# Kernel optimization log

Measured on AMD Instinct MI355X. Metric: run time of the kernel, lower is better.

Reference implementation:

```python
import jax, jax.numpy as jnp
import numpy as np

ALPHA = 0.01
EPSB = ALPHA / (1.0 - 2.0 * ALPHA)  # boundary_eps
BIG = 1e9  # stands in for +inf; all real boundary distances are << box diameter


def setup_inputs() -> dict:
    key = jax.random.key(0)
    ks = jax.random.split(key, 8)
    B, D, K = 32768, 16, 1024
    return {
        "x": jax.random.normal(ks[0], (B, D), jnp.float32),
        "logp": jnp.zeros((B, 1), jnp.float32),
        "an1_w": 0.1 * jax.random.normal(ks[1], (D,), jnp.float32),
        "an1_b": 0.1 * jax.random.normal(ks[2], (D,), jnp.float32),
        "an2_w": 0.1 * jax.random.normal(ks[3], (D,), jnp.float32),
        "an2_b": 0.1 * jax.random.normal(ks[4], (D,), jnp.float32),
        "shift_coeff": jax.random.normal(ks[5], (D,), jnp.float32),
        "anchor_raw": jax.random.normal(ks[6], (1, K, D), jnp.float32),  # vorproj._anchor_pts
        "box_min": -4.0 * jnp.ones((D,), jnp.float32),
        "box_max": 4.0 * jnp.ones((D,), jnp.float32),
        "mixture_logits": jnp.zeros((K,), jnp.float32),
    }


def reference(x, logp, an1_w, an1_b, an2_w, an2_b, shift_coeff,
              anchor_raw, box_min, box_max, mixture_logits):
    B, D = x.shape
    # --- actnorm1: y = (x + b) * exp(w); logdet = sum(w) ---
    x = (x + an1_b) * jnp.exp(an1_w)
    logp = logp - jnp.sum(an1_w)
    # --- logit_transform.inverse: y = (sigmoid(x) - alpha) / (1 - 2*alpha) ---
    ld = jnp.sum(jax.nn.log_sigmoid(x) + jax.nn.log_sigmoid(-x), axis=1, keepdims=True) \
         - D * jnp.log(1.0 - 2.0 * ALPHA)
    x = (jax.nn.sigmoid(x) - ALPHA) / (1.0 - 2.0 * ALPHA)
    logp = logp - ld
    # --- (-eps, 1+eps) -> (0, 1) ---
    span = 1.0 + 2.0 * EPSB
    x = (x + EPSB) / span
    logp = logp + D * jnp.log(span)
    # --- scale into box constraints ---
    scale = box_max - box_min  # (D,)
    x = x * scale + box_min
    logp = logp - jnp.sum(jnp.log(scale))
    # --- anchor points: R -> (-1,1) -> (0,1) -> box ---
    a = anchor_raw[0]                       # (K, D)
    a = a / (1.0 + jnp.abs(a))
    a = (a + 1.0) * 0.5 * scale + box_min   # (K, D)
    K = a.shape[0]
    # --- find_nearest: argmin_k ||x - a_k||^2 (drop const ||x||^2) ---
    a_sq = jnp.sum(a * a, axis=1)                    # (K,)
    d2 = a_sq[None, :] - 2.0 * (x @ a.T)             # (B, K)
    k = jnp.argmin(d2, axis=1)                       # (B,)
    mask = jax.nn.one_hot(k, K, dtype=bool).reshape(B, 1, K)
    x_k = a[k]                                       # (B, D) gathered anchor
    # --- shift toward anchor: x + c*(x_k - x); logdet = sum log(1-c) ---
    c = jax.nn.sigmoid(shift_coeff) * 0.98 + 0.01
    x = x + c * (x_k - x)
    logp = logp - jnp.sum(jnp.log1p(-c))
    # --- map_outside_cell: radial map of Voronoi cell (within box) onto R^D ---
    dx = x - x_k
    r = jnp.sqrt(jnp.sum(dx * dx, axis=1))           # (B,)
    u = dx / jnp.maximum(r, 1e-12)[:, None]          # (B, D) unit direction
    # half-plane boundary distance t_j = (||a_j - a_k||^2 / 2) / (u . (a_j - a_k))
    proj = u @ a.T - jnp.sum(u * x_k, axis=1, keepdims=True)              # (B, K)
    halfdist = 0.5 * (a_sq[None, :] + a_sq[k][:, None] - 2.0 * (x_k @ a.T))  # (B, K)
    self_mask = jnp.arange(K)[None, :] == k[:, None]
    valid = jnp.logical_and(jnp.logical_not(self_mask), proj > 1e-12)
    t_half = jnp.where(valid, halfdist / jnp.where(valid, proj, 1.0), BIG)
    # box-face distances along u
    up = u > 1e-12
    un = u < -1e-12
    t_box = jnp.where(up, (box_max[None, :] - x_k) / jnp.where(up, u, 1.0),
            jnp.where(un, (box_min[None, :] - x_k) / jnp.where(un, u, 1.0), BIG))
    t = jnp.minimum(jnp.min(t_half, axis=1), jnp.min(t_box, axis=1))      # (B,)
    ratio = r / t                                     # in [0, 0.99] after shift
    s = 1.0 / (1.0 - ratio)
    x = x_k + dx * s[:, None]
    # logdet = (D+1) * log(t / (t - r)) = -(D+1) * log1p(-ratio)
    logp = logp + (D + 1.0) * jnp.log1p(-ratio)[:, None]
    # --- subtract cell center ---
    x = x - x_k
    # --- actnorm2 ---
    x = (x + an2_b) * jnp.exp(an2_w)
    logp = logp - jnp.sum(an2_w)
    # --- mixture component log-prob ---
    logprobs = jax.nn.log_softmax(mixture_logits)
    logp = logp - logprobs[k][:, None]
    return x, logp, mask
```

## Files before the change

kernel.cpp:

```cpp
#include <hip/hip_runtime.h>
#include <math.h>

#define DD 16
#define KK 1024

#define WS_A    0
#define WS_ASQ  16384
#define WS_OMC  17408
#define WS_B2   17424
#define WS_E2   17440
#define WS_MN   17456
#define WS_MX   17472
#define WS_SCL  17488
#define WS_DIM  17504
#define WS_E1   17520
#define WS_BASE 17536
#define WS_TOTD 17537
#define WS_NEED_BYTES (WS_TOTD * 8)

__device__ __forceinline__ double xformD(double rv, double mn, double scl) {
  double t = rv / (1.0 + fabs(rv));
  return (t + 1.0) * 0.5 * scl + mn;
}
__device__ __forceinline__ float xformF(float v, float mn, float mx) {
  return (v / (1.f + fabsf(v)) + 1.f) * 0.5f * (mx - mn) + mn;
}

__global__ __launch_bounds__(256) void vor_pre(
    const float* __restrict__ an1_w, const float* __restrict__ an2_w,
    const float* __restrict__ an2_b, const float* __restrict__ shift_c,
    const float* __restrict__ anchor_raw,
    const float* __restrict__ box_min, const float* __restrict__ box_max,
    const float* __restrict__ mlogits, double* __restrict__ ws)
{
  __shared__ double redD[16];
  const int tid = threadIdx.x;
  const int blk = blockIdx.x;

  if (blk == 0 && tid < DD) {
    double w1 = (double)an1_w[tid], w2 = (double)an2_w[tid];
    double sgc = 1.0 / (1.0 + exp(-(double)shift_c[tid]));
    double c = sgc * 0.98 + 0.01;
    double mn = (double)box_min[tid], mx = (double)box_max[tid];
    ws[WS_OMC + tid] = 1.0 - c;
    ws[WS_B2  + tid] = (double)an2_b[tid];
    ws[WS_E2  + tid] = exp(w2);
    ws[WS_MN  + tid] = mn;
    ws[WS_MX  + tid] = mx;
    ws[WS_SCL + tid] = mx - mn;
    ws[WS_E1  + tid] = exp(w1);
    ws[WS_DIM + tid] = -w1 - log(mx - mn) - log1p(-c) - w2;
  }
  const int j0 = blk * 64;
  for (int e = tid; e < 64 * DD; e += 256) {
    int j = j0 + (e >> 4), d = e & 15;
    double mn = (double)box_min[d];
    double scl = (double)box_max[d] - mn;
    ws[WS_A + (size_t)j * DD + d] = xformD((double)anchor_raw[j * DD + d], mn, scl);
  }
  __syncthreads();
  for (int j = j0 + tid; j < j0 + 64; j += 256) {
    double s = 0.0;
    #pragma unroll
    for (int d = 0; d < DD; ++d) { double a = ws[WS_A + (size_t)j * DD + d]; s = fma(a, a, s); }
    ws[WS_ASQ + j] = s;
  }
  if (blk != 0) return;
  float lm = -3.4e38f;
  for (int i = tid; i < KK; i += 256) lm = fmaxf(lm, mlogits[i]);
  #pragma unroll
  for (int o = 32; o > 0; o >>= 1) lm = fmaxf(lm, __shfl_xor(lm, o));
  if ((tid & 63) == 0) redD[tid >> 6] = (double)lm;
  __syncthreads();
  float gmax = (float)fmax(fmax(redD[0], redD[1]), fmax(redD[2], redD[3]));
  double lsum = 0.0;
  for (int i = tid; i < KK; i += 256) lsum += exp((double)mlogits[i] - (double)gmax);
  #pragma unroll
  for (int o = 32; o > 0; o >>= 1) lsum += __shfl_xor(lsum, o);
  if ((tid & 63) == 0) redD[4 + (tid >> 6)] = lsum;
  __syncthreads();
  if (tid == 0) {
    double lse = (double)gmax + log(redD[4] + redD[5] + redD[6] + redD[7]);
    double b = (double)DD * (log(0.98) + log(1.0 + 2.0 * (0.01 / 0.98)));
    #pragma unroll
    for (int d = 0; d < DD; ++d) b += ws[WS_DIM + d];
    ws[WS_BASE] = b + lse;
  }
}

#define NT2 1024
#define RPB2 128
#define SL2 8
#define JSL2 (KK / SL2)

__global__ __launch_bounds__(NT2, 4) void vor4(
    const float* __restrict__ x_in, const float* __restrict__ logp_in,
    const float* __restrict__ an1_b,
    const float* __restrict__ mlogits, const double* __restrict__ ws,
    float* __restrict__ out, int Brows)
{
  __shared__ __align__(16) float sA[KK][DD];
  __shared__ float  sAsqH[KK];
  __shared__ double sX4D[DD][RPB2];
  __shared__ float  sLT[DD][RPB2];
  __shared__ double sD2[16][64];
  __shared__ int    sJJ[16][64];
  __shared__ float  sRat[16][64];
  __shared__ float  sOmcF[DD], sB2F[DD], sE2F[DD], sMnF[DD], sMxF[DD];

  const int tid  = threadIdx.x;
  const int w    = tid >> 6;
  const int lane = tid & 63;
  const int rg   = w >> 3;
  const int sl   = w & 7;
  const int rrow = rg * 64 + lane;
  const int row  = blockIdx.x * RPB2 + rrow;
  const size_t coreEnd = (size_t)Brows * (DD + 1);

  if (tid < DD) {
    sOmcF[tid] = (float)ws[WS_OMC + tid];
    sB2F[tid]  = (float)ws[WS_B2 + tid];
    sE2F[tid]  = (float)ws[WS_E2 + tid];
    sMnF[tid]  = (float)ws[WS_MN + tid];
    sMxF[tid]  = (float)ws[WS_MX + tid];
  }
  for (int e = tid; e < KK * DD / 4; e += NT2) {
    double2 p0 = ((const double2*)(ws + WS_A))[e * 2 + 0];
    double2 p1 = ((const double2*)(ws + WS_A))[e * 2 + 1];
    ((float4*)sA)[e] = make_float4((float)p0.x, (float)p0.y, (float)p1.x, (float)p1.y);
  }
  {
    const double A = 0.01, EPSB = 0.01 / 0.98;
    const double SPAN = 1.0 + 2.0 * EPSB;
    const float* xb = x_in + (size_t)blockIdx.x * RPB2 * DD;
    for (int e = tid; e < RPB2 * DD; e += NT2) {
      int rr = e >> 4, d = e & 15;
      double y1 = ((double)xb[e] + (double)an1_b[d]) * ws[WS_E1 + d];
      double sg = 1.0 / (1.0 + exp(-y1));
      double x2 = (sg - A) / (1.0 - 2.0 * A);
      double x3 = (x2 + EPSB) / SPAN;
      double x4 = x3 * ws[WS_SCL + d] + ws[WS_MN + d];
      sX4D[d][rr] = x4;
      double ay = fabs(y1);
      sLT[d][rr] = (float)(ay + 2.0 * log1p(exp(-ay)));
    }
  }
  {
    float4* mz = (float4*)(out + coreEnd + (size_t)blockIdx.x * RPB2 * KK);
    #pragma unroll 4
    for (int i = tid; i < RPB2 * KK / 4; i += NT2)
      mz[i] = make_float4(0.f, 0.f, 0.f, 0.f);
  }
  __syncthreads();

  for (int j = tid; j < KK; j += NT2) {
    float acc = 0.f;
    #pragma unroll
    for (int d = 0; d < DD; ++d) { float a = sA[j][d]; acc = fmaf(a, a, acc); }
    sAsqH[j] = 0.5f * acc;
  }

  float x4f[DD];
  #pragma unroll
  for (int d = 0; d < DD; ++d) x4f[d] = (float)sX4D[d][rrow];
  __syncthreads();

  const int jlo = sl * JSL2, jhi = jlo + JSL2;
  float m1 = -3.4e38f, m2v = -3.4e38f;
  int j1 = jlo, j2v = jlo;
  #pragma unroll 4
  for (int j = jlo; j < jhi; ++j) {
    const float4* ar = (const float4*)&sA[j][0];
    float4 a0 = ar[0], a1 = ar[1], a2 = ar[2], a3 = ar[3];
    float accA = -sAsqH[j], accB = 0.f;
    accA = fmaf(x4f[0],  a0.x, accA); accB = fmaf(x4f[8],  a2.x, accB);
    accA = fmaf(x4f[1],  a0.y, accA); accB = fmaf(x4f[9],  a2.y, accB);
    accA = fmaf(x4f[2],  a0.z, accA); accB = fmaf(x4f[10], a2.z, accB);
    accA = fmaf(x4f[3],  a0.w, accA); accB = fmaf(x4f[11], a2.w, accB);
    accA = fmaf(x4f[4],  a1.x, accA); accB = fmaf(x4f[12], a3.x, accB);
    accA = fmaf(x4f[5],  a1.y, accA); accB = fmaf(x4f[13], a3.y, accB);
    accA = fmaf(x4f[6],  a1.z, accA); accB = fmaf(x4f[14], a3.z, accB);
    accA = fmaf(x4f[7],  a1.w, accA); accB = fmaf(x4f[15], a3.w, accB);
    float acc = accA + accB;
    bool gt1 = acc > m1;
    bool gt2 = acc > m2v;
    m2v = gt1 ? m1 : (gt2 ? acc : m2v);
    j2v = gt1 ? j1 : (gt2 ? j : j2v);
    m1  = gt1 ? acc : m1;
    j1  = gt1 ? j : j1;
  }

  {
    double bestD = 1e300; int bk = 0x7fffffff;
    #pragma unroll
    for (int t = 0; t < 2; ++t) {
      int j = t ? j2v : j1;
      const double* aj = ws + WS_A + (size_t)j * DD;
      double dot = 0.0;
      #pragma unroll
      for (int d = 0; d < DD; ++d) dot = fma(sX4D[d][rrow], aj[d], dot);
      double d2 = ws[WS_ASQ + j] - 2.0 * dot;
      if (d2 < bestD || (d2 == bestD && j < bk)) { bestD = d2; bk = j; }
    }
    sD2[w][lane] = bestD;
    sJJ[w][lane] = bk;
  }
  __syncthreads();

  int k = 0x7fffffff;
  {
    double kb = 1e300;
    #pragma unroll
    for (int ss = 0; ss < SL2; ++ss) {
      double d = sD2[rg * 8 + ss][lane];
      int    j = sJJ[rg * 8 + ss][lane];
      if (d < kb || (d == kb && j < k)) { kb = d; k = j; }
    }
  }

  float akf[DD], dxf[DD];
  float r2f = 0.f, dxak = 0.f;
  #pragma unroll
  for (int d = 0; d < DD; ++d) {
    float a = sA[k][d];
    akf[d] = a;
    float dx = sOmcF[d] * (x4f[d] - a);
    dxf[d] = dx;
    r2f  = fmaf(dx, dx, r2f);
    dxak = fmaf(dx, a, dxak);
  }
  const float rf   = sqrtf(r2f);
  const float rrf  = fmaxf(rf, 1e-12f);
  const float scal = rf / rrf;
  const float epsr = 1e-12f * rf;
  const float asqhk = sAsqH[k];

  float q1 = 0.f, h1 = 1.f;
  #pragma unroll 2
  for (int j = jlo; j < jhi; ++j) {
    const float4* ar = (const float4*)&sA[j][0];
    float4 a0 = ar[0], a1 = ar[1], a2 = ar[2], a3 = ar[3];
    float qA = -dxak, qB = 0.f;
    float hA = asqhk + sAsqH[j], hB = 0.f;
    qA = fmaf(dxf[0],  a0.x, qA); qB = fmaf(dxf[8],  a2.x, qB);
    hA = fmaf(-akf[0], a0.x, hA); hB = fmaf(-akf[8], a2.x, hB);
    qA = fmaf(dxf[1],  a0.y, qA); qB = fmaf(dxf[9],  a2.y, qB);
    hA = fmaf(-akf[1], a0.y, hA); hB = fmaf(-akf[9], a2.y, hB);
    qA = fmaf(dxf[2],  a0.z, qA); qB = fmaf(dxf[10], a2.z, qB);
    hA = fmaf(-akf[2], a0.z, hA); hB = fmaf(-akf[10],a2.z, hB);
    qA = fmaf(dxf[3],  a0.w, qA); qB = fmaf(dxf[11], a2.w, qB);
    hA = fmaf(-akf[3], a0.w, hA); hB = fmaf(-akf[11],a2.w, hB);
    qA = fmaf(dxf[4],  a1.x, qA); qB = fmaf(dxf[12], a3.x, qB);
    hA = fmaf(-akf[4], a1.x, hA); hB = fmaf(-akf[12],a3.x, hB);
    qA = fmaf(dxf[5],  a1.y, qA); qB = fmaf(dxf[13], a3.y, qB);
    hA = fmaf(-akf[5], a1.y, hA); hB = fmaf(-akf[13],a3.y, hB);
    qA = fmaf(dxf[6],  a1.z, qA); qB = fmaf(dxf[14], a3.z, qB);
    hA = fmaf(-akf[6], a1.z, hA); hB = fmaf(-akf[14],a3.z, hB);
    qA = fmaf(dxf[7],  a1.w, qA); qB = fmaf(dxf[15], a3.w, qB);
    hA = fmaf(-akf[7], a1.w, hA); hB = fmaf(-akf[15],a3.w, hB);
    float q = qA + qB, h = hA + hB;
    bool upd = (j != k) & (q > epsr) & (q * h1 > q1 * h);
    q1 = upd ? q : q1;
    h1 = upd ? h : h1;
  }
  sRat[w][lane] = scal * (q1 / h1);
  __syncthreads();

  if (sl == 0) {
    float ratio = rf * 1e-9f;
    #pragma unroll
    for (int ss = 0; ss < SL2; ++ss) ratio = fmaxf(ratio, sRat[rg * 8 + ss][lane]);
    #pragma unroll
    for (int d = 0; d < DD; ++d) {
      float uf = dxf[d] / rrf;
      if (uf > 1e-12f)        ratio = fmaxf(ratio, rf * uf / (sMxF[d] - akf[d]));
      else if (uf < -1e-12f)  ratio = fmaxf(ratio, rf * uf / (sMnF[d] - akf[d]));
    }
    float sS = 1.0f / (1.0f - ratio);
    float xo[DD];
    float lsig = 0.f;
    #pragma unroll
    for (int d = 0; d < DD; ++d) {
      xo[d] = (dxf[d] * sS + sB2F[d]) * sE2F[d];
      lsig += sLT[d][rrow];
    }
    float4* xp = (float4*)(out + (size_t)row * DD);
    xp[0] = make_float4(xo[0], xo[1], xo[2], xo[3]);
    xp[1] = make_float4(xo[4], xo[5], xo[6], xo[7]);
    xp[2] = make_float4(xo[8], xo[9], xo[10], xo[11]);
    xp[3] = make_float4(xo[12], xo[13], xo[14], xo[15]);
    double lp = (double)logp_in[row] + ws[WS_BASE] + (double)lsig
              + 17.0 * log1p(-(double)ratio)
              - (double)mlogits[k];
    out[(size_t)Brows * DD + row] = (float)lp;
    out[coreEnd + (size_t)row * KK + k] = 1.0f;
  }
}

#define NT 256
#define RPB 64
#define SLC4 4
#define JSL4 (KK / SLC4)

__global__ __launch_bounds__(NT, 2) void vor_green(
    const float* __restrict__ x_in, const float* __restrict__ logp_in,
    const float* __restrict__ an1_w, const float* __restrict__ an1_b,
    const float* __restrict__ an2_w, const float* __restrict__ an2_b,
    const float* __restrict__ shift_c, const float* __restrict__ anchor_raw,
    const float* __restrict__ box_min, const float* __restrict__ box_max,
    const float* __restrict__ mlogits,
    float* __restrict__ out, int Brows)
{
  __shared__ __align__(16) float sA[KK][DD];
  __shared__ float  sAsqH[KK];
  __shared__ float  sX4T[DD][RPB];
  __shared__ int    sPj1[SLC4][RPB], sPj2[SLC4][RPB];
  __shared__ int    sRI1[SLC4][RPB], sRI2[SLC4][RPB];
  __shared__ double sPartD[8];
  __shared__ double sE1D[DD], sB1D[DD], sOmcD[DD], sB2D[DD], sE2D[DD];
  __shared__ double sMnD[DD], sMxD[DD], sSclD[DD], sDimD[DD];
  __shared__ double sBaseD;
  __shared__ int    sKidx[RPB];

  const int tid  = threadIdx.x;
  const int sl   = tid >> 6;
  const int lane = tid & 63;
  const int row  = blockIdx.x * RPB + lane;
  const size_t coreEnd = (size_t)Brows * (DD + 1);

  for (int e = tid; e < KK * DD / 4; e += NT) {
    float4 raw = ((const float4*)anchor_raw)[e];
    float4 bmn = ((const float4*)box_min)[e & 3];
    float4 bmx = ((const float4*)box_max)[e & 3];
    float4 o;
    o.x = xformF(raw.x, bmn.x, bmx.x);
    o.y = xformF(raw.y, bmn.y, bmx.y);
    o.z = xformF(raw.z, bmn.z, bmx.z);
    o.w = xformF(raw.w, bmn.w, bmx.w);
    ((float4*)sA)[e] = o;
  }
  if (tid < DD) {
    double w1 = (double)an1_w[tid];
    sE1D[tid] = exp(w1);
    sB1D[tid] = (double)an1_b[tid];
    double sgc = 1.0 / (1.0 + exp(-(double)shift_c[tid]));
    double c = sgc * 0.98 + 0.01;
    sOmcD[tid] = 1.0 - c;
    double mn = (double)box_min[tid], mx = (double)box_max[tid];
    sMnD[tid] = mn; sMxD[tid] = mx; sSclD[tid] = mx - mn;
    double w2 = (double)an2_w[tid];
    sE2D[tid] = exp(w2);
    sB2D[tid] = (double)an2_b[tid];
    sDimD[tid] = -w1 - log(mx - mn) - log1p(-c) - w2;
  }
  __syncthreads();

  for (int j = tid; j < KK; j += NT) {
    float acc = 0.f;
    #pragma unroll
    for (int d = 0; d < DD; ++d) { float a = sA[j][d]; acc = fmaf(a, a, acc); }
    sAsqH[j] = 0.5f * acc;
  }

  float lm = -3.4e38f;
  for (int i = tid; i < KK; i += NT) lm = fmaxf(lm, mlogits[i]);
  #pragma unroll
  for (int o = 32; o > 0; o >>= 1) lm = fmaxf(lm, __shfl_xor(lm, o));
  if (lane == 0) sPartD[sl] = (double)lm;
  __syncthreads();
  float gmax = (float)fmax(fmax(sPartD[0], sPartD[1]), fmax(sPartD[2], sPartD[3]));
  double lsum = 0.0;
  for (int i = tid; i < KK; i += NT) lsum += exp((double)mlogits[i] - (double)gmax);
  #pragma unroll
  for (int o = 32; o > 0; o >>= 1) lsum += __shfl_xor(lsum, o);
  if (lane == 0) sPartD[4 + sl] = lsum;
  __syncthreads();
  if (tid == 0) {
    double lse = (double)gmax + log(sPartD[4] + sPartD[5] + sPartD[6] + sPartD[7]);
    double b = (double)DD * (log(0.98) + log(1.0 + 2.0 * (0.01 / 0.98)));
    #pragma unroll
    for (int d = 0; d < DD; ++d) b += sDimD[d];
    sBaseD = b + lse;
  }

  double x4d[DD];
  double lsigD = 0.0;
  if (sl == 0) {
    const double A = 0.01, EPSB = 0.01 / 0.98;
    const double SPAN = 1.0 + 2.0 * EPSB;
    const float* xr = x_in + (size_t)row * DD;
    #pragma unroll
    for (int d = 0; d < DD; ++d) {
      double y1 = ((double)xr[d] + sB1D[d]) * sE1D[d];
      double sg = 1.0 / (1.0 + exp(-y1));
      double x2 = (sg - A) / (1.0 - 2.0 * A);
      double x3 = (x2 + EPSB) / SPAN;
      double x4 = x3 * sSclD[d] + sMnD[d];
      x4d[d] = x4;
      sX4T[d][lane] = (float)x4;
      double ay = fabs(y1);
      lsigD += ay + 2.0 * log1p(exp(-ay));
    }
  }
  {
    float4* mz = (float4*)(out + coreEnd + (size_t)blockIdx.x * RPB * KK);
    #pragma unroll 4
    for (int i = tid; i < RPB * KK / 4; i += NT)
      mz[i] = make_float4(0.f, 0.f, 0.f, 0.f);
  }
  __syncthreads();

  float x4f[DD];
  #pragma unroll
  for (int d = 0; d < DD; ++d) x4f[d] = sX4T[d][lane];

  float m1 = -3.4e38f, m2v = -3.4e38f;
  int j1 = 0x7fffffff, j2v = 0x7fffffff;
  const int jlo = sl * JSL4, jhi = jlo + JSL4;
  #pragma unroll 2
  for (int j = jlo; j < jhi; ++j) {
    float acc = -sAsqH[j];
    const float4* ar = (const float4*)&sA[j][0];
    #pragma unroll
    for (int dq = 0; dq < 4; ++dq) {
      float4 a4 = ar[dq];
      acc = fmaf(x4f[4 * dq + 0], a4.x, acc);
      acc = fmaf(x4f[4 * dq + 1], a4.y, acc);
      acc = fmaf(x4f[4 * dq + 2], a4.z, acc);
      acc = fmaf(x4f[4 * dq + 3], a4.w, acc);
    }
    bool gt1 = acc > m1;
    bool gt2 = acc > m2v;
    m2v = gt1 ? m1 : (gt2 ? acc : m2v);
    j2v = gt1 ? j1 : (gt2 ? j : j2v);
    m1  = gt1 ? acc : m1;
    j1  = gt1 ? j : j1;
  }
  sPj1[sl][lane] = j1;
  sPj2[sl][lane] = j2v;
  __syncthreads();

  if (sl == 0) {
    double best = 1e300; int bk = 0x7fffffff;
    #pragma unroll
    for (int ss = 0; ss < SLC4; ++ss) {
      #pragma unroll
      for (int t = 0; t < 2; ++t) {
        int j = t ? sPj2[ss][lane] : sPj1[ss][lane];
        double asq = 0.0, dot = 0.0;
        #pragma unroll
        for (int d = 0; d < DD; ++d) {
          double a = xformD((double)anchor_raw[j * DD + d], sMnD[d], sSclD[d]);
          asq = fma(a, a, asq);
          dot = fma(x4d[d], a, dot);
        }
        double d2 = asq - 2.0 * dot;
        if (d2 < best || (d2 == best && j < bk)) { best = d2; bk = j; }
      }
    }
    sKidx[lane] = bk;
  }
  __syncthreads();

  const int k = sKidx[lane];

  float akf[DD], dxf[DD];
  float r2f = 0.f, dxak = 0.f;
  #pragma unroll
  for (int d = 0; d < DD; ++d) {
    float a = sA[k][d];
    akf[d] = a;
    float dx = (float)sOmcD[d] * (x4f[d] - a);
    dxf[d] = dx;
    r2f  = fmaf(dx, dx, r2f);
    dxak = fmaf(dx, a, dxak);
  }
  const float epsr = 1e-12f * sqrtf(r2f);
  const float asqhk = sAsqH[k];

  float q1 = 0.f, h1 = 1.f, q2 = 0.f, h2 = 1.f;
  int i1 = -1, i2 = -1;
  #pragma unroll 2
  for (int j = jlo; j < jhi; ++j) {
    float q = -dxak;
    float h = asqhk + sAsqH[j];
    const float4* ar = (const float4*)&sA[j][0];
    #pragma unroll
    for (int dq = 0; dq < 4; ++dq) {
      float4 a4 = ar[dq];
      q = fmaf(dxf[4 * dq + 0], a4.x, q);
      q = fmaf(dxf[4 * dq + 1], a4.y, q);
      q = fmaf(dxf[4 * dq + 2], a4.z, q);
      q = fmaf(dxf[4 * dq + 3], a4.w, q);
      h = fmaf(-akf[4 * dq + 0], a4.x, h);
      h = fmaf(-akf[4 * dq + 1], a4.y, h);
      h = fmaf(-akf[4 * dq + 2], a4.z, h);
      h = fmaf(-akf[4 * dq + 3], a4.w, h);
    }
    bool valid = (j != k) & (q > epsr);
    bool b1 = valid && (q * h1 > q1 * h);
    bool b2 = valid && (q * h2 > q2 * h);
    float nq2 = b1 ? q1 : (b2 ? q : q2);
    float nh2 = b1 ? h1 : (b2 ? h : h2);
    int   ni2 = b1 ? i1 : (b2 ? j : i2);
    q1 = b1 ? q : q1; h1 = b1 ? h : h1; i1 = b1 ? j : i1;
    q2 = nq2; h2 = nh2; i2 = ni2;
  }
  sRI1[sl][lane] = i1;
  sRI2[sl][lane] = i2;
  __syncthreads();

  if (sl == 0) {
    double akD[DD], dxD[DD];
    double r2 = 0.0;
    #pragma unroll
    for (int d = 0; d < DD; ++d) {
      double a = xformD((double)anchor_raw[k * DD + d], sMnD[d], sSclD[d]);
      akD[d] = a;
      double dx = sOmcD[d] * (x4d[d] - a);
      dxD[d] = dx;
      r2 = fma(dx, dx, r2);
    }
    double rD = sqrt(r2);
    double rr = fmax(rD, 1e-12);
    double ratio = rD / 1e9;

    #pragma unroll
    for (int ss = 0; ss < SLC4; ++ss) {
      #pragma unroll
      for (int t = 0; t < 2; ++t) {
        int j = t ? sRI2[ss][lane] : sRI1[ss][lane];
        if (j < 0 || j == k) continue;
        double q = 0.0, h = 0.0;
        #pragma unroll
        for (int d = 0; d < DD; ++d) {
          double aj = xformD((double)anchor_raw[j * DD + d], sMnD[d], sSclD[d]);
          double g = aj - akD[d];
          q = fma(dxD[d], g, q);
          h = fma(g, g, h);
        }
        double proj = q / rr;
        if (proj > 1e-12) {
          double cand = rD * proj / (0.5 * h);
          ratio = fmax(ratio, cand);
        }
      }
    }
    #pragma unroll
    for (int d = 0; d < DD; ++d) {
      double u = dxD[d] / rr;
      if (u > 1e-12)        ratio = fmax(ratio, rD * u / (sMxD[d] - akD[d]));
      else if (u < -1e-12)  ratio = fmax(ratio, rD * u / (sMnD[d] - akD[d]));
    }

    double sS = 1.0 / (1.0 - ratio);
    float* xo = out + (size_t)row * DD;
    #pragma unroll
    for (int d = 0; d < DD; ++d) {
      double x7 = dxD[d] * sS;
      double x8 = (x7 + sB2D[d]) * sE2D[d];
      xo[d] = (float)x8;
    }
    double lp = (double)logp_in[row] + sBaseD + lsigD
              + 17.0 * log1p(-ratio)
              - (double)mlogits[k];
    out[(size_t)Brows * DD + row] = (float)lp;
    out[coreEnd + (size_t)row * KK + k] = 1.0f;
  }
}

extern "C" void kernel_launch(void* const* d_in, const int* in_sizes, int n_in,
                              void* d_out, int out_size, void* d_ws, size_t ws_size,
                              hipStream_t stream) {
  (void)n_in; (void)out_size;
  const float* x_in   = (const float*)d_in[0];
  const float* logp   = (const float*)d_in[1];
  const float* an1w   = (const float*)d_in[2];
  const float* an1b   = (const float*)d_in[3];
  const float* an2w   = (const float*)d_in[4];
  const float* an2b   = (const float*)d_in[5];
  const float* shiftc = (const float*)d_in[6];
  const float* anchor = (const float*)d_in[7];
  const float* bmin   = (const float*)d_in[8];
  const float* bmax   = (const float*)d_in[9];
  const float* mlog   = (const float*)d_in[10];
  const int B = in_sizes[0] / DD;

  if (ws_size >= (size_t)WS_NEED_BYTES && d_ws != nullptr && (B % RPB2) == 0) {
    double* ws = (double*)d_ws;
    hipLaunchKernelGGL(vor_pre, dim3(16), dim3(256), 0, stream,
                       an1w, an2w, an2b, shiftc, anchor, bmin, bmax, mlog, ws);
    hipLaunchKernelGGL(vor4, dim3(B / RPB2), dim3(NT2), 0, stream,
                       x_in, logp, an1b, mlog,
                       (const double*)ws, (float*)d_out, B);
  } else {
    hipLaunchKernelGGL(vor_green, dim3(B / RPB), dim3(NT), 0, stream,
                       x_in, logp, an1w, an1b, an2w, an2b, shiftc, anchor,
                       bmin, bmax, mlog, (float*)d_out, B);
  }
}
```

Before: 104.2 us.

## Precompute float anchors in workspace and read them via uniform global loads

The pre-kernel now also writes single-precision anchor coordinates and half squared norms into the workspace. The main kernel stops staging the full 1024x16 anchor table into LDS, shrinks to 512 threads and 64 rows per block, and reads anchors through wave-uniform global loads that may become scalar loads. This removes the per-block LDS fill, its conversion and a barrier, and lowers LDS use so more blocks can be resident. In exchange every block re-reads the anchor table from cache, and there are twice as many blocks.

```diff
diff --git a/kernel.cpp b/kernel.cpp
--- a/kernel.cpp
+++ b/kernel.cpp
@@ -15,7 +15,9 @@
 #define WS_DIM  17504
 #define WS_E1   17520
 #define WS_BASE 17536
-#define WS_TOTD 17537
+#define WS_AF   17538
+#define WS_ASQF 25730
+#define WS_TOTD 26242
 #define WS_NEED_BYTES (WS_TOTD * 8)
 
 __device__ __forceinline__ double xformD(double rv, double mn, double scl) {
@@ -36,6 +38,8 @@
   __shared__ double redD[16];
   const int tid = threadIdx.x;
   const int blk = blockIdx.x;
+  float* aF    = (float*)(ws + WS_AF);
+  float* asqHF = (float*)(ws + WS_ASQF);
 
   if (blk == 0 && tid < DD) {
     double w1 = (double)an1_w[tid], w2 = (double)an2_w[tid];
@@ -61,9 +65,19 @@
   __syncthreads();
   for (int j = j0 + tid; j < j0 + 64; j += 256) {
     double s = 0.0;
-    #pragma unroll
-    for (int d = 0; d < DD; ++d) { double a = ws[WS_A + (size_t)j * DD + d]; s = fma(a, a, s); }
+    float af[DD];
+    float accf = 0.f;
+    #pragma unroll
+    for (int d = 0; d < DD; ++d) {
+      double a = ws[WS_A + (size_t)j * DD + d];
+      s = fma(a, a, s);
+      af[d] = (float)a;
+      accf = fmaf(af[d], af[d], accf);
+    }
     ws[WS_ASQ + j] = s;
+    asqHF[j] = 0.5f * accf;
+    #pragma unroll
+    for (int d = 0; d < DD; ++d) aF[j * DD + d] = af[d];
   }
   if (blk != 0) return;
   float lm = -3.4e38f;
@@ -88,33 +102,29 @@
   }
 }
 
-#define NT2 1024
-#define RPB2 128
-#define SL2 8
-#define JSL2 (KK / SL2)
-
-__global__ __launch_bounds__(NT2, 4) void vor4(
+#define NT5 512
+#define RPB5 64
+#define SL5 8
+#define JSL5 (KK / SL5)
+
+__global__ __launch_bounds__(NT5, 4) void vor5(
     const float* __restrict__ x_in, const float* __restrict__ logp_in,
-    const float* __restrict__ an1_b,
-    const float* __restrict__ mlogits, const double* __restrict__ ws,
+    const float* __restrict__ an1_b, const float* __restrict__ mlogits,
+    const double* __restrict__ ws,
+    const float* __restrict__ aF, const float* __restrict__ asqHF,
     float* __restrict__ out, int Brows)
 {
-  __shared__ __align__(16) float sA[KK][DD];
-  __shared__ float  sAsqH[KK];
-  __shared__ double sX4D[DD][RPB2];
-  __shared__ float  sLT[DD][RPB2];
-  __shared__ double sD2[16][64];
-  __shared__ int    sJJ[16][64];
-  __shared__ float  sRat[16][64];
+  __shared__ double sX4D[DD][RPB5];
+  __shared__ float  sLT[DD][RPB5];
+  __shared__ double sD2[SL5][RPB5];
+  __shared__ int    sJJ[SL5][RPB5];
+  __shared__ float  sRat[SL5][RPB5];
   __shared__ float  sOmcF[DD], sB2F[DD], sE2F[DD], sMnF[DD], sMxF[DD];
 
   const int tid  = threadIdx.x;
-  const int w    = tid >> 6;
+  const int sl   = tid >> 6;
   const int lane = tid & 63;
-  const int rg   = w >> 3;
-  const int sl   = w & 7;
-  const int rrow = rg * 64 + lane;
-  const int row  = blockIdx.x * RPB2 + rrow;
+  const int row  = blockIdx.x * RPB5 + lane;
   const size_t coreEnd = (size_t)Brows * (DD + 1);
 
   if (tid < DD) {
@@ -124,16 +134,11 @@
     sMnF[tid]  = (float)ws[WS_MN + tid];
     sMxF[tid]  = (float)ws[WS_MX + tid];
   }
-  for (int e = tid; e < KK * DD / 4; e += NT2) {
-    double2 p0 = ((const double2*)(ws + WS_A))[e * 2 + 0];
-    double2 p1 = ((const double2*)(ws + WS_A))[e * 2 + 1];
-    ((float4*)sA)[e] = make_float4((float)p0.x, (float)p0.y, (float)p1.x, (float)p1.y);
-  }
   {
     const double A = 0.01, EPSB = 0.01 / 0.98;
     const double SPAN = 1.0 + 2.0 * EPSB;
-    const float* xb = x_in + (size_t)blockIdx.x * RPB2 * DD;
-    for (int e = tid; e < RPB2 * DD; e += NT2) {
+    const float* xb = x_in + (size_t)blockIdx.x * RPB5 * DD;
+    for (int e = tid; e < RPB5 * DD; e += NT5) {
       int rr = e >> 4, d = e & 15;
       double y1 = ((double)xb[e] + (double)an1_b[d]) * ws[WS_E1 + d];
       double sg = 1.0 / (1.0 + exp(-y1));
@@ -146,41 +151,32 @@
     }
   }
   {
-    float4* mz = (float4*)(out + coreEnd + (size_t)blockIdx.x * RPB2 * KK);
+    float4* mz = (float4*)(out + coreEnd + (size_t)blockIdx.x * RPB5 * KK);
     #pragma unroll 4
-    for (int i = tid; i < RPB2 * KK / 4; i += NT2)
+    for (int i = tid; i < RPB5 * KK / 4; i += NT5)
       mz[i] = make_float4(0.f, 0.f, 0.f, 0.f);
   }
   __syncthreads();
 
-  for (int j = tid; j < KK; j += NT2) {
-    float acc = 0.f;
-    #pragma unroll
-    for (int d = 0; d < DD; ++d) { float a = sA[j][d]; acc = fmaf(a, a, acc); }
-    sAsqH[j] = 0.5f * acc;
-  }
-
   float x4f[DD];
   #pragma unroll
-  for (int d = 0; d < DD; ++d) x4f[d] = (float)sX4D[d][rrow];
-  __syncthreads();
-
-  const int jlo = sl * JSL2, jhi = jlo + JSL2;
+  for (int d = 0; d < DD; ++d) x4f[d] = (float)sX4D[d][lane];
+
+  const int jlo = sl * JSL5, jhi = jlo + JSL5;
   float m1 = -3.4e38f, m2v = -3.4e38f;
   int j1 = jlo, j2v = jlo;
   #pragma unroll 4
   for (int j = jlo; j < jhi; ++j) {
-    const float4* ar = (const float4*)&sA[j][0];
-    float4 a0 = ar[0], a1 = ar[1], a2 = ar[2], a3 = ar[3];
-    float accA = -sAsqH[j], accB = 0.f;
-    accA = fmaf(x4f[0],  a0.x, accA); accB = fmaf(x4f[8],  a2.x, accB);
-    accA = fmaf(x4f[1],  a0.y, accA); accB = fmaf(x4f[9],  a2.y, accB);
-    accA = fmaf(x4f[2],  a0.z, accA); accB = fmaf(x4f[10], a2.z, accB);
-    accA = fmaf(x4f[3],  a0.w, accA); accB = fmaf(x4f[11], a2.w, accB);
-    accA = fmaf(x4f[4],  a1.x, accA); accB = fmaf(x4f[12], a3.x, accB);
-    accA = fmaf(x4f[5],  a1.y, accA); accB = fmaf(x4f[13], a3.y, accB);
-    accA = fmaf(x4f[6],  a1.z, accA); accB = fmaf(x4f[14], a3.z, accB);
-    accA = fmaf(x4f[7],  a1.w, accA); accB = fmaf(x4f[15], a3.w, accB);
+    const float* ar = aF + j * DD;
+    float accA = -asqHF[j], accB = 0.f;
+    accA = fmaf(x4f[0],  ar[0],  accA); accB = fmaf(x4f[8],  ar[8],  accB);
+    accA = fmaf(x4f[1],  ar[1],  accA); accB = fmaf(x4f[9],  ar[9],  accB);
+    accA = fmaf(x4f[2],  ar[2],  accA); accB = fmaf(x4f[10], ar[10], accB);
+    accA = fmaf(x4f[3],  ar[3],  accA); accB = fmaf(x4f[11], ar[11], accB);
+    accA = fmaf(x4f[4],  ar[4],  accA); accB = fmaf(x4f[12], ar[12], accB);
+    accA = fmaf(x4f[5],  ar[5],  accA); accB = fmaf(x4f[13], ar[13], accB);
+    accA = fmaf(x4f[6],  ar[6],  accA); accB = fmaf(x4f[14], ar[14], accB);
+    accA = fmaf(x4f[7],  ar[7],  accA); accB = fmaf(x4f[15], ar[15], accB);
     float acc = accA + accB;
     bool gt1 = acc > m1;
     bool gt2 = acc > m2v;
@@ -198,12 +194,12 @@
       const double* aj = ws + WS_A + (size_t)j * DD;
       double dot = 0.0;
       #pragma unroll
-      for (int d = 0; d < DD; ++d) dot = fma(sX4D[d][rrow], aj[d], dot);
+      for (int d = 0; d < DD; ++d) dot = fma(sX4D[d][lane], aj[d], dot);
       double d2 = ws[WS_ASQ + j] - 2.0 * dot;
       if (d2 < bestD || (d2 == bestD && j < bk)) { bestD = d2; bk = j; }
     }
-    sD2[w][lane] = bestD;
-    sJJ[w][lane] = bk;
+    sD2[sl][lane] = bestD;
+    sJJ[sl][lane] = bk;
   }
   __syncthreads();
 
@@ -211,65 +207,66 @@
   {
     double kb = 1e300;
     #pragma unroll
-    for (int ss = 0; ss < SL2; ++ss) {
-      double d = sD2[rg * 8 + ss][lane];
-      int    j = sJJ[rg * 8 + ss][lane];
+    for (int ss = 0; ss < SL5; ++ss) {
+      double d = sD2[ss][lane];
+      int    j = sJJ[ss][lane];
       if (d < kb || (d == kb && j < k)) { kb = d; k = j; }
     }
   }
 
-  float akf[DD], dxf[DD];
+  const float4* akp = (const float4*)(aF + (size_t)k * DD);
+  float4 k0 = akp[0], k1 = akp[1], k2 = akp[2], k3 = akp[3];
+  float akf[DD] = {k0.x,k0.y,k0.z,k0.w, k1.x,k1.y,k1.z,k1.w,
+                   k2.x,k2.y,k2.z,k2.w, k3.x,k3.y,k3.z,k3.w};
+  float dxf[DD];
   float r2f = 0.f, dxak = 0.f;
   #pragma unroll
   for (int d = 0; d < DD; ++d) {
-    float a = sA[k][d];
-    akf[d] = a;
-    float dx = sOmcF[d] * (x4f[d] - a);
+    float dx = sOmcF[d] * (x4f[d] - akf[d]);
     dxf[d] = dx;
     r2f  = fmaf(dx, dx, r2f);
-    dxak = fmaf(dx, a, dxak);
+    dxak = fmaf(dx, akf[d], dxak);
   }
   const float rf   = sqrtf(r2f);
   const float rrf  = fmaxf(rf, 1e-12f);
   const float scal = rf / rrf;
   const float epsr = 1e-12f * rf;
-  const float asqhk = sAsqH[k];
+  const float asqhk = asqHF[k];
 
   float q1 = 0.f, h1 = 1.f;
   #pragma unroll 2
   for (int j = jlo; j < jhi; ++j) {
-    const float4* ar = (const float4*)&sA[j][0];
-    float4 a0 = ar[0], a1 = ar[1], a2 = ar[2], a3 = ar[3];
+    const float* ar = aF + j * DD;
     float qA = -dxak, qB = 0.f;
-    float hA = asqhk + sAsqH[j], hB = 0.f;
-    qA = fmaf(dxf[0],  a0.x, qA); qB = fmaf(dxf[8],  a2.x, qB);
-    hA = fmaf(-akf[0], a0.x, hA); hB = fmaf(-akf[8], a2.x, hB);
-    qA = fmaf(dxf[1],  a0.y, qA); qB = fmaf(dxf[9],  a2.y, qB);
-    hA = fmaf(-akf[1], a0.y, hA); hB = fmaf(-akf[9], a2.y, hB);
-    qA = fmaf(dxf[2],  a0.z, qA); qB = fmaf(dxf[10], a2.z, qB);
-    hA = fmaf(-akf[2], a0.z, hA); hB = fmaf(-akf[10],a2.z, hB);
-    qA = fmaf(dxf[3],  a0.w, qA); qB = fmaf(dxf[11], a2.w, qB);
-    hA = fmaf(-akf[3], a0.w, hA); hB = fmaf(-akf[11],a2.w, hB);
-    qA = fmaf(dxf[4],  a1.x, qA); qB = fmaf(dxf[12], a3.x, qB);
-    hA = fmaf(-akf[4], a1.x, hA); hB = fmaf(-akf[12],a3.x, hB);
-    qA = fmaf(dxf[5],  a1.y, qA); qB = fmaf(dxf[13], a3.y, qB);
-    hA = fmaf(-akf[5], a1.y, hA); hB = fmaf(-akf[13],a3.y, hB);
-    qA = fmaf(dxf[6],  a1.z, qA); qB = fmaf(dxf[14], a3.z, qB);
-    hA = fmaf(-akf[6], a1.z, hA); hB = fmaf(-akf[14],a3.z, hB);
-    qA = fmaf(dxf[7],  a1.w, qA); qB = fmaf(dxf[15], a3.w, qB);
-    hA = fmaf(-akf[7], a1.w, hA); hB = fmaf(-akf[15],a3.w, hB);
+    float hA = asqhk + asqHF[j], hB = 0.f;
+    qA = fmaf(dxf[0],  ar[0],  qA); qB = fmaf(dxf[8],  ar[8],  qB);
+    hA = fmaf(-akf[0], ar[0],  hA); hB = fmaf(-akf[8], ar[8],  hB);
+    qA = fmaf(dxf[1],  ar[1],  qA); qB = fmaf(dxf[9],  ar[9],  qB);
+    hA = fmaf(-akf[1], ar[1],  hA); hB = fmaf(-akf[9], ar[9],  hB);
+    qA = fmaf(dxf[2],  ar[2],  qA); qB = fmaf(dxf[10], ar[10], qB);
+    hA = fmaf(-akf[2], ar[2],  hA); hB = fmaf(-akf[10],ar[10], hB);
+    qA = fmaf(dxf[3],  ar[3],  qA); qB = fmaf(dxf[11], ar[11], qB);
+    hA = fmaf(-akf[3], ar[3],  hA); hB = fmaf(-akf[11],ar[11], hB);
+    qA = fmaf(dxf[4],  ar[4],  qA); qB = fmaf(dxf[12], ar[12], qB);
+    hA = fmaf(-akf[4], ar[4],  hA); hB = fmaf(-akf[12],ar[12], hB);
+    qA = fmaf(dxf[5],  ar[5],  qA); qB = fmaf(dxf[13], ar[13], qB);
+    hA = fmaf(-akf[5], ar[5],  hA); hB = fmaf(-akf[13],ar[13], hB);
+    qA = fmaf(dxf[6],  ar[6],  qA); qB = fmaf(dxf[14], ar[14], qB);
+    hA = fmaf(-akf[6], ar[6],  hA); hB = fmaf(-akf[14],ar[14], hB);
+    qA = fmaf(dxf[7],  ar[7],  qA); qB = fmaf(dxf[15], ar[15], qB);
+    hA = fmaf(-akf[7], ar[7],  hA); hB = fmaf(-akf[15],ar[15], hB);
     float q = qA + qB, h = hA + hB;
     bool upd = (j != k) & (q > epsr) & (q * h1 > q1 * h);
     q1 = upd ? q : q1;
     h1 = upd ? h : h1;
   }
-  sRat[w][lane] = scal * (q1 / h1);
+  sRat[sl][lane] = scal * (q1 / h1);
   __syncthreads();
 
   if (sl == 0) {
     float ratio = rf * 1e-9f;
     #pragma unroll
-    for (int ss = 0; ss < SL2; ++ss) ratio = fmaxf(ratio, sRat[rg * 8 + ss][lane]);
+    for (int ss = 0; ss < SL5; ++ss) ratio = fmaxf(ratio, sRat[ss][lane]);
     #pragma unroll
     for (int d = 0; d < DD; ++d) {
       float uf = dxf[d] / rrf;
@@ -282,7 +279,7 @@
     #pragma unroll
     for (int d = 0; d < DD; ++d) {
       xo[d] = (dxf[d] * sS + sB2F[d]) * sE2F[d];
-      lsig += sLT[d][rrow];
+      lsig += sLT[d][lane];
     }
     float4* xp = (float4*)(out + (size_t)row * DD);
     xp[0] = make_float4(xo[0], xo[1], xo[2], xo[3]);
@@ -586,13 +583,15 @@
   const float* mlog   = (const float*)d_in[10];
   const int B = in_sizes[0] / DD;
 
-  if (ws_size >= (size_t)WS_NEED_BYTES && d_ws != nullptr && (B % RPB2) == 0) {
+  if (ws_size >= (size_t)WS_NEED_BYTES && d_ws != nullptr && (B % RPB5) == 0) {
     double* ws = (double*)d_ws;
+    const float* aF    = (const float*)(ws + WS_AF);
+    const float* asqHF = (const float*)(ws + WS_ASQF);
     hipLaunchKernelGGL(vor_pre, dim3(16), dim3(256), 0, stream,
                        an1w, an2w, an2b, shiftc, anchor, bmin, bmax, mlog, ws);
-    hipLaunchKernelGGL(vor4, dim3(B / RPB2), dim3(NT2), 0, stream,
-                       x_in, logp, an1b, mlog,
-                       (const double*)ws, (float*)d_out, B);
+    hipLaunchKernelGGL(vor5, dim3(B / RPB5), dim3(NT5), 0, stream,
+                       x_in, logp, an1b, mlog, (const double*)ws,
+                       aF, asqHF, (float*)d_out, B);
   } else {
     hipLaunchKernelGGL(vor_green, dim3(B / RPB), dim3(NT), 0, stream,
                        x_in, logp, an1w, an1b, an2w, an2b, shiftc, anchor,
```

After: 167.7 us. 60.9% more time.
